# Kernel tuning notes

Measured on AMD Instinct MI355X. Metric: run time of the kernel, lower is better.

The kernel has to match this reference:

```python
import jax, jax.numpy as jnp
import numpy as np

N_NODES = 100000


def gcn_layer(x, W, b, src, dst, n):
    # PyG GCNConv: h = x @ W, then D^{-1/2}(A+I)D^{-1/2} aggregation, then + b
    h = x @ W  # [N, out]
    ones = jnp.ones(src.shape[0], dtype=h.dtype)
    deg = jax.ops.segment_sum(ones, dst, num_segments=n) + 1.0  # +1 for self loop
    dinv = jax.lax.rsqrt(deg)  # [N]
    norm = dinv[src] * dinv[dst]  # [E]
    msgs = h[src] * norm[:, None]  # gather + scale, [E, out]
    agg = jax.ops.segment_sum(msgs, dst, num_segments=n)
    agg = agg + h * (dinv * dinv)[:, None]  # self-loop term
    return agg + b


def setup_inputs() -> dict:
    key = jax.random.key(0)
    k1, k2, k3, k4, k5, k6 = jax.random.split(key, 6)
    in_dim, h1, h2 = 256, 128, 64
    x = jax.random.normal(k1, (N_NODES, in_dim), dtype=jnp.float32)
    edge_index = jax.random.randint(k2, (2, 1600000), 0, N_NODES, dtype=jnp.int64)
    # Glorot-style init for weights, zeros for bias (PyG default)
    W1 = jax.random.normal(k3, (in_dim, h1), dtype=jnp.float32) / np.sqrt(in_dim)
    b1 = jnp.zeros((h1,), dtype=jnp.float32)
    W2 = jax.random.normal(k4, (h1, h2), dtype=jnp.float32) / np.sqrt(h1)
    b2 = jnp.zeros((h2,), dtype=jnp.float32)
    return {"x": x, "W1": W1, "b1": b1, "W2": W2, "b2": b2, "edge_index": edge_index}


def reference(x, W1, b1, W2, b2, edge_index):
    src, dst = edge_index[0], edge_index[1]
    n = x.shape[0]
    h = jax.nn.relu(gcn_layer(x, W1, b1, src, dst, n))
    h = jax.nn.relu(gcn_layer(h, W2, b2, src, dst, n))
    return h
```

## Files before the change

### kernel.cpp

```cpp
#include <hip/hip_runtime.h>
#include <hip/hip_bf16.h>


typedef __attribute__((ext_vector_type(8))) short bf16x8;
typedef __attribute__((ext_vector_type(4))) float f32x4;

__device__ inline unsigned short f2bf(float f) {
    unsigned u = __float_as_uint(f);
    u = (u + 0x7fff + ((u >> 16) & 1)) >> 16;
    return (unsigned short)u;
}
__device__ inline float bf2f(unsigned short h) {
    return __uint_as_float(((unsigned)h) << 16);
}
__device__ inline float bflo(unsigned u) { return __uint_as_float(u << 16); }
__device__ inline float bfhi(unsigned u) { return __uint_as_float(u & 0xffff0000u); }
__device__ inline unsigned pack_bf16_2(float lo, float hi) {
    return (unsigned)f2bf(lo) | ((unsigned)f2bf(hi) << 16);
}
__device__ inline void cvt8(const float* v, bf16x8& h8, bf16x8& l8) {
    #pragma unroll
    for (int j = 0; j < 8; ++j) {
        unsigned short h = f2bf(v[j]);
        h8[j] = (short)h;
        l8[j] = (short)f2bf(v[j] - bf2f(h));
    }
}

__global__ void prep_kernel(const int* __restrict__ dst, int* __restrict__ deg, int E,
        const float* __restrict__ W1, unsigned short* __restrict__ w1h,
        unsigned short* __restrict__ w1l,
        const float* __restrict__ W2, unsigned short* __restrict__ w2h,
        unsigned short* __restrict__ w2l) {
    const int W1B = (256 * 128) / 256;
    const int W2B = (128 * 64) / 256;
    int b = blockIdx.x;
    if (b < W1B) {
        int idx = b * 256 + threadIdx.x;
        int k = idx >> 7, n = idx & 127;
        float v = W1[idx];
        unsigned short h = f2bf(v);
        w1h[(size_t)n * 256 + k] = h;
        w1l[(size_t)n * 256 + k] = f2bf(v - bf2f(h));
    } else if (b < W1B + W2B) {
        int idx = (b - W1B) * 256 + threadIdx.x;
        int k = idx >> 6, n = idx & 63;
        float v = W2[idx];
        unsigned short h = f2bf(v);
        w2h[(size_t)n * 128 + k] = h;
        w2l[(size_t)n * 128 + k] = f2bf(v - bf2f(h));
    } else {
        int nb = gridDim.x - (W1B + W2B);
        int stride = nb * 256;
        for (int i = (b - W1B - W2B) * 256 + threadIdx.x; i < E; i += stride)
            atomicAdd(&deg[dst[i]], 1);
    }
}

__global__ __launch_bounds__(1024) void scan_partial_kernel(const int* __restrict__ deg,
        int* __restrict__ psum, float* __restrict__ dinv, int n) {
    __shared__ int wsum[16];
    int tid = threadIdx.x, wave = tid >> 6, lane = tid & 63;
    int i0 = blockIdx.x * 4096 + tid * 4;
    int v0 = 0, v1 = 0, v2 = 0, v3 = 0;
    if (i0 + 3 < n) {
        int4 v = *(const int4*)(deg + i0);
        v0 = v.x; v1 = v.y; v2 = v.z; v3 = v.w;
    } else {
        if (i0 + 0 < n) v0 = deg[i0 + 0];
        if (i0 + 1 < n) v1 = deg[i0 + 1];
        if (i0 + 2 < n) v2 = deg[i0 + 2];
        if (i0 + 3 < n) v3 = deg[i0 + 3];
    }
    if (i0 + 0 < n) dinv[i0 + 0] = 1.0f / sqrtf((float)v0 + 1.0f);
    if (i0 + 1 < n) dinv[i0 + 1] = 1.0f / sqrtf((float)v1 + 1.0f);
    if (i0 + 2 < n) dinv[i0 + 2] = 1.0f / sqrtf((float)v2 + 1.0f);
    if (i0 + 3 < n) dinv[i0 + 3] = 1.0f / sqrtf((float)v3 + 1.0f);
    int s = v0 + v1 + v2 + v3;
    #pragma unroll
    for (int off = 1; off < 64; off <<= 1) s += __shfl_xor(s, off, 64);
    if (lane == 0) wsum[wave] = s;
    __syncthreads();
    if (tid == 0) {
        int t = 0;
        #pragma unroll
        for (int w = 0; w < 16; ++w) t += wsum[w];
        psum[blockIdx.x] = t;
    }
}

__global__ __launch_bounds__(1024) void scan_local_kernel(const int* __restrict__ deg,
        const int* __restrict__ psum, int* __restrict__ offs, int n, int sb) {
    __shared__ int wsum[16];
    int tid = threadIdx.x, wave = tid >> 6, lane = tid & 63;
    int bid = blockIdx.x;
    int base = 0, total = 0;
    for (int w = 0; w < sb; ++w) {
        int t = psum[w];
        if (w < bid) base += t;
        total += t;
    }
    if (bid == 0 && tid == 0) offs[n] = total;

    int i0 = bid * 4096 + tid * 4;
    int v0 = 0, v1 = 0, v2 = 0, v3 = 0;
    if (i0 + 3 < n) {
        int4 v = *(const int4*)(deg + i0);
        v0 = v.x; v1 = v.y; v2 = v.z; v3 = v.w;
    } else {
        if (i0 + 0 < n) v0 = deg[i0 + 0];
        if (i0 + 1 < n) v1 = deg[i0 + 1];
        if (i0 + 2 < n) v2 = deg[i0 + 2];
        if (i0 + 3 < n) v3 = deg[i0 + 3];
    }
    int s = v0 + v1 + v2 + v3;
    int x = s;
    #pragma unroll
    for (int off = 1; off < 64; off <<= 1) {
        int y = __shfl_up(x, off, 64);
        if (lane >= off) x += y;
    }
    if (lane == 63) wsum[wave] = x;
    __syncthreads();
    int wbase = 0;
    #pragma unroll
    for (int w = 0; w < 16; ++w)
        if (w < wave) wbase += wsum[w];
    int ex = base + wbase + (x - s);
    if (i0 + 0 < n) offs[i0 + 0] = ex;
    if (i0 + 1 < n) offs[i0 + 1] = ex + v0;
    if (i0 + 2 < n) offs[i0 + 2] = ex + v0 + v1;
    if (i0 + 3 < n) offs[i0 + 3] = ex + v0 + v1 + v2;
}

__global__ __launch_bounds__(256) void fused_fill_gemm1(
        const int* __restrict__ src, const int* __restrict__ dst,
        const int* __restrict__ offs, int* __restrict__ cursor,
        int* __restrict__ csr, int E, int NG,
        const float* __restrict__ X,
        const unsigned short* __restrict__ Wh, const unsigned short* __restrict__ Wl,
        const float* __restrict__ dinv, unsigned short* __restrict__ G, int M) {
    const int bid2 = blockIdx.x >> 1;
    if (!(blockIdx.x & 1)) {
        int stride = NG * 256;
        for (int i = bid2 * 256 + threadIdx.x; i < E; i += stride) {
            int d = dst[i];
            int pos = offs[d] + atomicAdd(&cursor[d], 1);
            csr[pos] = src[i];
        }
        return;
    }
    constexpr int K = 256;
    const int tid = threadIdx.x;
    const int wv = tid >> 6, ln = tid & 63;
    const int l16 = ln & 15, kseg = ln >> 4;
    const int r0 = bid2 * 128 + wv * 32;

    int rA0 = r0 + l16;       if (rA0 >= M) rA0 = M - 1;
    int rA1 = r0 + 16 + l16;  if (rA1 >= M) rA1 = M - 1;
    const float* pA0 = X + (size_t)rA0 * K + kseg * 8;
    const float* pA1 = X + (size_t)rA1 * K + kseg * 8;

    f32x4 acc[2][8];
    #pragma unroll
    for (int a = 0; a < 2; ++a)
        #pragma unroll
        for (int b = 0; b < 8; ++b) acc[a][b] = 0;

    #pragma unroll 2
    for (int k0 = 0; k0 < K; k0 += 32) {
        bf16x8 ah[2], al[2];
        {
            float4 qa = *(const float4*)(pA0 + k0);
            float4 qb = *(const float4*)(pA0 + k0 + 4);
            float v[8] = {qa.x, qa.y, qa.z, qa.w, qb.x, qb.y, qb.z, qb.w};
            cvt8(v, ah[0], al[0]);
        }
        {
            float4 qa = *(const float4*)(pA1 + k0);
            float4 qb = *(const float4*)(pA1 + k0 + 4);
            float v[8] = {qa.x, qa.y, qa.z, qa.w, qb.x, qb.y, qb.z, qb.w};
            cvt8(v, ah[1], al[1]);
        }
        #pragma unroll
        for (int tc = 0; tc < 8; ++tc) {
            size_t wo = (size_t)(tc * 16 + l16) * K + k0 + kseg * 8;
            bf16x8 bh = *(const bf16x8*)(Wh + wo);
            bf16x8 bl = *(const bf16x8*)(Wl + wo);
            #pragma unroll
            for (int tr = 0; tr < 2; ++tr) {
                acc[tr][tc] = __builtin_amdgcn_mfma_f32_16x16x32_bf16(ah[tr], bh, acc[tr][tc], 0, 0, 0);
                acc[tr][tc] = __builtin_amdgcn_mfma_f32_16x16x32_bf16(al[tr], bh, acc[tr][tc], 0, 0, 0);
                acc[tr][tc] = __builtin_amdgcn_mfma_f32_16x16x32_bf16(ah[tr], bl, acc[tr][tc], 0, 0, 0);
            }
        }
    }

    #pragma unroll
    for (int tr = 0; tr < 2; ++tr) {
        int rbase = r0 + tr * 16 + (ln >> 4) * 4;
        #pragma unroll
        for (int r = 0; r < 4; ++r) {
            int row = rbase + r;
            if (row < M) {
                float dv = dinv[row];
                #pragma unroll
                for (int tc = 0; tc < 8; ++tc)
                    G[(size_t)row * 128 + tc * 16 + l16] = f2bf(acc[tr][tc][r] * dv);
            }
        }
    }
}

__global__ __launch_bounds__(256) void gemm2_kernel(const unsigned short* __restrict__ H,
        const unsigned short* __restrict__ Wh, const unsigned short* __restrict__ Wl,
        const float* __restrict__ dinv, unsigned short* __restrict__ G, int M) {
    constexpr int K = 128;
    const int tid = threadIdx.x;
    const int wv = tid >> 6, ln = tid & 63;
    const int l16 = ln & 15, kseg = ln >> 4;
    const int r0 = blockIdx.x * 128 + wv * 32;

    int rA0 = r0 + l16;       if (rA0 >= M) rA0 = M - 1;
    int rA1 = r0 + 16 + l16;  if (rA1 >= M) rA1 = M - 1;
    const unsigned short* pA0 = H + (size_t)rA0 * K + kseg * 8;
    const unsigned short* pA1 = H + (size_t)rA1 * K + kseg * 8;

    f32x4 acc[2][4];
    #pragma unroll
    for (int a = 0; a < 2; ++a)
        #pragma unroll
        for (int b = 0; b < 4; ++b) acc[a][b] = 0;

    #pragma unroll
    for (int k0 = 0; k0 < K; k0 += 32) {
        bf16x8 a0 = *(const bf16x8*)(pA0 + k0);
        bf16x8 a1 = *(const bf16x8*)(pA1 + k0);
        #pragma unroll
        for (int tc = 0; tc < 4; ++tc) {
            size_t wo = (size_t)(tc * 16 + l16) * K + k0 + kseg * 8;
            bf16x8 bh = *(const bf16x8*)(Wh + wo);
            bf16x8 bl = *(const bf16x8*)(Wl + wo);
            acc[0][tc] = __builtin_amdgcn_mfma_f32_16x16x32_bf16(a0, bh, acc[0][tc], 0, 0, 0);
            acc[0][tc] = __builtin_amdgcn_mfma_f32_16x16x32_bf16(a0, bl, acc[0][tc], 0, 0, 0);
            acc[1][tc] = __builtin_amdgcn_mfma_f32_16x16x32_bf16(a1, bh, acc[1][tc], 0, 0, 0);
            acc[1][tc] = __builtin_amdgcn_mfma_f32_16x16x32_bf16(a1, bl, acc[1][tc], 0, 0, 0);
        }
    }

    #pragma unroll
    for (int tr = 0; tr < 2; ++tr) {
        int rbase = r0 + tr * 16 + (ln >> 4) * 4;
        #pragma unroll
        for (int r = 0; r < 4; ++r) {
            int row = rbase + r;
            if (row < M) {
                float dv = dinv[row];
                #pragma unroll
                for (int tc = 0; tc < 4; ++tc)
                    G[(size_t)row * 64 + tc * 16 + l16] = f2bf(acc[tr][tc][r] * dv);
            }
        }
    }
}

__global__ __launch_bounds__(256) void aggregate128_kernel(const unsigned* __restrict__ G,
        const int* __restrict__ csr, const int* __restrict__ offs,
        const float* __restrict__ dinv, const float* __restrict__ bias,
        unsigned* __restrict__ out, int n) {
    int wave = threadIdx.x >> 6, lane = threadIdx.x & 63;
    int node = blockIdx.x * 4 + wave;
    if (node >= n) return;
    int beg = offs[node], end = offs[node + 1];

    unsigned u = G[(size_t)node * 64 + lane];
    float a0 = bflo(u), a1 = bfhi(u);
    int e = beg;
    for (; e + 4 <= end; e += 4) {
        int s0 = csr[e], s1 = csr[e + 1], s2 = csr[e + 2], s3 = csr[e + 3];
        unsigned u0 = G[(size_t)s0 * 64 + lane];
        unsigned u1 = G[(size_t)s1 * 64 + lane];
        unsigned u2 = G[(size_t)s2 * 64 + lane];
        unsigned u3 = G[(size_t)s3 * 64 + lane];
        a0 += (bflo(u0) + bflo(u1)) + (bflo(u2) + bflo(u3));
        a1 += (bfhi(u0) + bfhi(u1)) + (bfhi(u2) + bfhi(u3));
    }
    for (; e < end; ++e) {
        unsigned u0 = G[(size_t)csr[e] * 64 + lane];
        a0 += bflo(u0);
        a1 += bfhi(u0);
    }
    float di = dinv[node];
    float rx = fmaxf(fmaf(a0, di, bias[lane * 2 + 0]), 0.0f);
    float ry = fmaxf(fmaf(a1, di, bias[lane * 2 + 1]), 0.0f);
    out[(size_t)node * 64 + lane] = pack_bf16_2(rx, ry);
}

__global__ __launch_bounds__(256) void aggregate64_kernel(const unsigned* __restrict__ G,
        const int* __restrict__ csr, const int* __restrict__ offs,
        const float* __restrict__ dinv, const float* __restrict__ bias,
        float* __restrict__ out, int n) {
    int wave = threadIdx.x >> 6, lane = threadIdx.x & 63;
    int node = blockIdx.x * 4 + wave;
    if (node >= n) return;
    int beg = offs[node], end = offs[node + 1];
    int half = lane >> 5, col = lane & 31;

    float a0 = 0.0f, a1 = 0.0f;
    if (half == 0) {
        unsigned u = G[(size_t)node * 32 + col];
        a0 = bflo(u); a1 = bfhi(u);
    }
    int e = beg;
    for (; e + 4 <= end; e += 4) {
        int sA = csr[e + half], sB = csr[e + 2 + half];
        unsigned uA = G[(size_t)sA * 32 + col];
        unsigned uB = G[(size_t)sB * 32 + col];
        a0 += bflo(uA) + bflo(uB);
        a1 += bfhi(uA) + bfhi(uB);
    }
    if (e + 2 <= end) {
        int sA = csr[e + half];
        unsigned uA = G[(size_t)sA * 32 + col];
        a0 += bflo(uA);
        a1 += bfhi(uA);
        e += 2;
    }
    if (e < end && half == 0) {
        unsigned uA = G[(size_t)csr[e] * 32 + col];
        a0 += bflo(uA);
        a1 += bfhi(uA);
    }
    a0 += __shfl_down(a0, 32, 64);
    a1 += __shfl_down(a1, 32, 64);
    if (half == 0) {
        float di = dinv[node];
        float2 r;
        r.x = fmaxf(fmaf(a0, di, bias[col * 2 + 0]), 0.0f);
        r.y = fmaxf(fmaf(a1, di, bias[col * 2 + 1]), 0.0f);
        ((float2*)(out + (size_t)node * 64))[col] = r;
    }
}

extern "C" void kernel_launch(void* const* d_in, const int* in_sizes, int n_in,
                              void* d_out, int out_size, void* d_ws, size_t ws_size,
                              hipStream_t stream) {
    const float* x  = (const float*)d_in[0];
    const float* W1 = (const float*)d_in[1];
    const float* b1 = (const float*)d_in[2];
    const float* W2 = (const float*)d_in[3];
    const float* b2 = (const float*)d_in[4];
    const int* edge = (const int*)d_in[5];

    const int IN = 256, H1 = 128, H2 = 64;
    const int E = in_sizes[5] / 2;
    const int N = in_sizes[0] / IN;
    const int* srcp = edge;
    const int* dstp = edge + E;

    char* ws = (char*)d_ws;
    auto alignup = [](size_t v) { return (v + 255) & ~(size_t)255; };
    size_t off = 0;
    size_t degSz = alignup((size_t)N * 4);
    int*            deg    = (int*)(ws + off);            off += degSz;
    int*            cursor = (int*)(ws + off);            off += degSz;
    int*            offs   = (int*)(ws + off);            off += alignup(((size_t)N + 1) * 4);
    float*          dinv   = (float*)(ws + off);          off += degSz;
    int*            psum   = (int*)(ws + off);            off += alignup(64 * 4);
    int*            csr    = (int*)(ws + off);            off += alignup((size_t)E * 4);
    unsigned short* wt1h   = (unsigned short*)(ws + off); off += alignup((size_t)IN * H1 * 2);
    unsigned short* wt1l   = (unsigned short*)(ws + off); off += alignup((size_t)IN * H1 * 2);
    unsigned short* wt2h   = (unsigned short*)(ws + off); off += alignup((size_t)H1 * H2 * 2);
    unsigned short* wt2l   = (unsigned short*)(ws + off); off += alignup((size_t)H1 * H2 * 2);
    unsigned short* g1     = (unsigned short*)(ws + off); off += alignup((size_t)N * H1 * 2);
    unsigned*       h1b    = (unsigned*)(ws + off);       off += alignup((size_t)N * (H1 / 2) * 4);
    unsigned short* g2     = g1;

    hipMemsetAsync(deg, 0, 2 * degSz, stream);

    int hgrid = 2048;
    int sb = (N + 4095) / 4096;

    prep_kernel<<<160 + hgrid, 256, 0, stream>>>(dstp, deg, E, W1, wt1h, wt1l,
                                                 W2, wt2h, wt2l);
    scan_partial_kernel<<<sb, 1024, 0, stream>>>(deg, psum, dinv, N);
    scan_local_kernel<<<sb, 1024, 0, stream>>>(deg, psum, offs, N, sb);

    const int NG = (N + 127) / 128;
    fused_fill_gemm1<<<2 * NG, 256, 0, stream>>>(srcp, dstp, offs, cursor, csr, E,
                                                 NG, x, wt1h, wt1l, dinv, g1, N);

    int agrid = (N + 3) / 4;
    aggregate128_kernel<<<agrid, 256, 0, stream>>>((const unsigned*)g1, csr, offs,
                                                   dinv, b1, h1b, N);
    gemm2_kernel<<<NG, 256, 0, stream>>>((const unsigned short*)h1b, wt2h, wt2l,
                                         dinv, g2, N);
    aggregate64_kernel<<<agrid, 256, 0, stream>>>((const unsigned*)g2, csr, offs,
                                                  dinv, b2, (float*)d_out, N);
}
```

Before: 544.0 us.

## Split fill from GEMM1, shrink GEMM tiles, deepen aggregation gather unroll

The fused CSR-fill and GEMM1 kernel becomes two kernels: a grid-stride fill kernel and a separate GEMM1. The GEMM1 block tile drops to 64 rows, with waves split across column halves and A loads prefetched one k-step ahead. GEMM2 also uses 64-row blocks with one 16-row tile per wave. Both aggregation kernels issue 8 neighbor gathers per iteration to raise memory-level parallelism. This gives up the overlap between fill atomics and GEMM compute in exchange for more blocks and better latency hiding, and adds one extra launch.

```diff
diff --git a/kernel.cpp b/kernel.cpp
--- a/kernel.cpp
+++ b/kernel.cpp
@@ -133,58 +133,63 @@
     if (i0 + 3 < n) offs[i0 + 3] = ex + v0 + v1 + v2;
 }
 
-__global__ __launch_bounds__(256) void fused_fill_gemm1(
-        const int* __restrict__ src, const int* __restrict__ dst,
+__global__ void fill_kernel(const int* __restrict__ src, const int* __restrict__ dst,
         const int* __restrict__ offs, int* __restrict__ cursor,
-        int* __restrict__ csr, int E, int NG,
-        const float* __restrict__ X,
+        int* __restrict__ csr, int E) {
+    int stride = gridDim.x * blockDim.x;
+    for (int i = blockIdx.x * blockDim.x + threadIdx.x; i < E; i += stride) {
+        int d = dst[i];
+        int pos = offs[d] + atomicAdd(&cursor[d], 1);
+        csr[pos] = src[i];
+    }
+}
+
+__global__ __launch_bounds__(256) void gemm1_kernel(const float* __restrict__ X,
         const unsigned short* __restrict__ Wh, const unsigned short* __restrict__ Wl,
         const float* __restrict__ dinv, unsigned short* __restrict__ G, int M) {
-    const int bid2 = blockIdx.x >> 1;
-    if (!(blockIdx.x & 1)) {
-        int stride = NG * 256;
-        for (int i = bid2 * 256 + threadIdx.x; i < E; i += stride) {
-            int d = dst[i];
-            int pos = offs[d] + atomicAdd(&cursor[d], 1);
-            csr[pos] = src[i];
-        }
-        return;
-    }
     constexpr int K = 256;
     const int tid = threadIdx.x;
     const int wv = tid >> 6, ln = tid & 63;
     const int l16 = ln & 15, kseg = ln >> 4;
-    const int r0 = bid2 * 128 + wv * 32;
+    const int wr = wv >> 1, wc = wv & 1;
+    const int r0 = blockIdx.x * 64 + wr * 32;
 
     int rA0 = r0 + l16;       if (rA0 >= M) rA0 = M - 1;
     int rA1 = r0 + 16 + l16;  if (rA1 >= M) rA1 = M - 1;
     const float* pA0 = X + (size_t)rA0 * K + kseg * 8;
     const float* pA1 = X + (size_t)rA1 * K + kseg * 8;
 
-    f32x4 acc[2][8];
+    f32x4 acc[2][4];
     #pragma unroll
     for (int a = 0; a < 2; ++a)
         #pragma unroll
-        for (int b = 0; b < 8; ++b) acc[a][b] = 0;
+        for (int b = 0; b < 4; ++b) acc[a][b] = 0;
+
+    float4 qa0 = *(const float4*)(pA0);
+    float4 qb0 = *(const float4*)(pA0 + 4);
+    float4 qa1 = *(const float4*)(pA1);
+    float4 qb1 = *(const float4*)(pA1 + 4);
 
     #pragma unroll 2
     for (int k0 = 0; k0 < K; k0 += 32) {
         bf16x8 ah[2], al[2];
         {
-            float4 qa = *(const float4*)(pA0 + k0);
-            float4 qb = *(const float4*)(pA0 + k0 + 4);
-            float v[8] = {qa.x, qa.y, qa.z, qa.w, qb.x, qb.y, qb.z, qb.w};
+            float v[8] = {qa0.x, qa0.y, qa0.z, qa0.w, qb0.x, qb0.y, qb0.z, qb0.w};
             cvt8(v, ah[0], al[0]);
         }
         {
-            float4 qa = *(const float4*)(pA1 + k0);
-            float4 qb = *(const float4*)(pA1 + k0 + 4);
-            float v[8] = {qa.x, qa.y, qa.z, qa.w, qb.x, qb.y, qb.z, qb.w};
+            float v[8] = {qa1.x, qa1.y, qa1.z, qa1.w, qb1.x, qb1.y, qb1.z, qb1.w};
             cvt8(v, ah[1], al[1]);
         }
-        #pragma unroll
-        for (int tc = 0; tc < 8; ++tc) {
-            size_t wo = (size_t)(tc * 16 + l16) * K + k0 + kseg * 8;
+        if (k0 + 32 < K) {
+            qa0 = *(const float4*)(pA0 + k0 + 32);
+            qb0 = *(const float4*)(pA0 + k0 + 36);
+            qa1 = *(const float4*)(pA1 + k0 + 32);
+            qb1 = *(const float4*)(pA1 + k0 + 36);
+        }
+        #pragma unroll
+        for (int tc = 0; tc < 4; ++tc) {
+            size_t wo = (size_t)(wc * 64 + tc * 16 + l16) * K + k0 + kseg * 8;
             bf16x8 bh = *(const bf16x8*)(Wh + wo);
             bf16x8 bl = *(const bf16x8*)(Wl + wo);
             #pragma unroll
@@ -205,8 +210,9 @@
             if (row < M) {
                 float dv = dinv[row];
                 #pragma unroll
-                for (int tc = 0; tc < 8; ++tc)
-                    G[(size_t)row * 128 + tc * 16 + l16] = f2bf(acc[tr][tc][r] * dv);
+                for (int tc = 0; tc < 4; ++tc)
+                    G[(size_t)row * 128 + wc * 64 + tc * 16 + l16] =
+                        f2bf(acc[tr][tc][r] * dv);
             }
         }
     }
@@ -219,38 +225,30 @@
     const int tid = threadIdx.x;
     const int wv = tid >> 6, ln = tid & 63;
     const int l16 = ln & 15, kseg = ln >> 4;
-    const int r0 = blockIdx.x * 128 + wv * 32;
-
-    int rA0 = r0 + l16;       if (rA0 >= M) rA0 = M - 1;
-    int rA1 = r0 + 16 + l16;  if (rA1 >= M) rA1 = M - 1;
+    const int r0 = blockIdx.x * 64 + wv * 16;
+
+    int rA0 = r0 + l16;  if (rA0 >= M) rA0 = M - 1;
     const unsigned short* pA0 = H + (size_t)rA0 * K + kseg * 8;
-    const unsigned short* pA1 = H + (size_t)rA1 * K + kseg * 8;
-
-    f32x4 acc[2][4];
-    #pragma unroll
-    for (int a = 0; a < 2; ++a)
-        #pragma unroll
-        for (int b = 0; b < 4; ++b) acc[a][b] = 0;
+
+    f32x4 acc[4];
+    #pragma unroll
+    for (int b = 0; b < 4; ++b) acc[b] = 0;
 
     #pragma unroll
     for (int k0 = 0; k0 < K; k0 += 32) {
         bf16x8 a0 = *(const bf16x8*)(pA0 + k0);
-        bf16x8 a1 = *(const bf16x8*)(pA1 + k0);
         #pragma unroll
         for (int tc = 0; tc < 4; ++tc) {
             size_t wo = (size_t)(tc * 16 + l16) * K + k0 + kseg * 8;
             bf16x8 bh = *(const bf16x8*)(Wh + wo);
             bf16x8 bl = *(const bf16x8*)(Wl + wo);
-            acc[0][tc] = __builtin_amdgcn_mfma_f32_16x16x32_bf16(a0, bh, acc[0][tc], 0, 0, 0);
-            acc[0][tc] = __builtin_amdgcn_mfma_f32_16x16x32_bf16(a0, bl, acc[0][tc], 0, 0, 0);
-            acc[1][tc] = __builtin_amdgcn_mfma_f32_16x16x32_bf16(a1, bh, acc[1][tc], 0, 0, 0);
-            acc[1][tc] = __builtin_amdgcn_mfma_f32_16x16x32_bf16(a1, bl, acc[1][tc], 0, 0, 0);
-        }
-    }
-
-    #pragma unroll
-    for (int tr = 0; tr < 2; ++tr) {
-        int rbase = r0 + tr * 16 + (ln >> 4) * 4;
+            acc[tc] = __builtin_amdgcn_mfma_f32_16x16x32_bf16(a0, bh, acc[tc], 0, 0, 0);
+            acc[tc] = __builtin_amdgcn_mfma_f32_16x16x32_bf16(a0, bl, acc[tc], 0, 0, 0);
+        }
+    }
+
+    {
+        int rbase = r0 + (ln >> 4) * 4;
         #pragma unroll
         for (int r = 0; r < 4; ++r) {
             int row = rbase + r;
@@ -258,7 +256,7 @@
                 float dv = dinv[row];
                 #pragma unroll
                 for (int tc = 0; tc < 4; ++tc)
-                    G[(size_t)row * 64 + tc * 16 + l16] = f2bf(acc[tr][tc][r] * dv);
+                    G[(size_t)row * 64 + tc * 16 + l16] = f2bf(acc[tc][r] * dv);
             }
         }
     }
@@ -276,14 +274,19 @@
     unsigned u = G[(size_t)node * 64 + lane];
     float a0 = bflo(u), a1 = bfhi(u);
     int e = beg;
+    for (; e + 8 <= end; e += 8) {
+        unsigned uu[8];
+        #pragma unroll
+        for (int j = 0; j < 8; ++j) uu[j] = G[(size_t)csr[e + j] * 64 + lane];
+        #pragma unroll
+        for (int j = 0; j < 8; ++j) { a0 += bflo(uu[j]); a1 += bfhi(uu[j]); }
+    }
     for (; e + 4 <= end; e += 4) {
-        int s0 = csr[e], s1 = csr[e + 1], s2 = csr[e + 2], s3 = csr[e + 3];
-        unsigned u0 = G[(size_t)s0 * 64 + lane];
-        unsigned u1 = G[(size_t)s1 * 64 + lane];
-        unsigned u2 = G[(size_t)s2 * 64 + lane];
-        unsigned u3 = G[(size_t)s3 * 64 + lane];
-        a0 += (bflo(u0) + bflo(u1)) + (bflo(u2) + bflo(u3));
-        a1 += (bfhi(u0) + bfhi(u1)) + (bfhi(u2) + bfhi(u3));
+        unsigned uu[4];
+        #pragma unroll
+        for (int j = 0; j < 4; ++j) uu[j] = G[(size_t)csr[e + j] * 64 + lane];
+        #pragma unroll
+        for (int j = 0; j < 4; ++j) { a0 += bflo(uu[j]); a1 += bfhi(uu[j]); }
     }
     for (; e < end; ++e) {
         unsigned u0 = G[(size_t)csr[e] * 64 + lane];
@@ -312,19 +315,17 @@
         a0 = bflo(u); a1 = bfhi(u);
     }
     int e = beg;
-    for (; e + 4 <= end; e += 4) {
-        int sA = csr[e + half], sB = csr[e + 2 + half];
-        unsigned uA = G[(size_t)sA * 32 + col];
-        unsigned uB = G[(size_t)sB * 32 + col];
-        a0 += bflo(uA) + bflo(uB);
-        a1 += bfhi(uA) + bfhi(uB);
-    }
-    if (e + 2 <= end) {
-        int sA = csr[e + half];
-        unsigned uA = G[(size_t)sA * 32 + col];
+    for (; e + 8 <= end; e += 8) {
+        unsigned uu[4];
+        #pragma unroll
+        for (int j = 0; j < 4; ++j) uu[j] = G[(size_t)csr[e + 2 * j + half] * 32 + col];
+        #pragma unroll
+        for (int j = 0; j < 4; ++j) { a0 += bflo(uu[j]); a1 += bfhi(uu[j]); }
+    }
+    for (; e + 2 <= end; e += 2) {
+        unsigned uA = G[(size_t)csr[e + half] * 32 + col];
         a0 += bflo(uA);
         a1 += bfhi(uA);
-        e += 2;
     }
     if (e < end && half == 0) {
         unsigned uA = G[(size_t)csr[e] * 32 + col];
@@ -378,23 +379,22 @@
 
     hipMemsetAsync(deg, 0, 2 * degSz, stream);
 
-    int hgrid = 2048;
     int sb = (N + 4095) / 4096;
 
-    prep_kernel<<<160 + hgrid, 256, 0, stream>>>(dstp, deg, E, W1, wt1h, wt1l,
-                                                 W2, wt2h, wt2l);
+    prep_kernel<<<160 + 2048, 256, 0, stream>>>(dstp, deg, E, W1, wt1h, wt1l,
+                                                W2, wt2h, wt2l);
     scan_partial_kernel<<<sb, 1024, 0, stream>>>(deg, psum, dinv, N);
     scan_local_kernel<<<sb, 1024, 0, stream>>>(deg, psum, offs, N, sb);
-
-    const int NG = (N + 127) / 128;
-    fused_fill_gemm1<<<2 * NG, 256, 0, stream>>>(srcp, dstp, offs, cursor, csr, E,
-                                                 NG, x, wt1h, wt1l, dinv, g1, N);
-
+    fill_kernel<<<1024, 256, 0, stream>>>(srcp, dstp, offs, cursor, csr, E);
+
+    int g64 = (N + 63) / 64;
     int agrid = (N + 3) / 4;
+
+    gemm1_kernel<<<g64, 256, 0, stream>>>(x, wt1h, wt1l, dinv, g1, N);
     aggregate128_kernel<<<agrid, 256, 0, stream>>>((const unsigned*)g1, csr, offs,
                                                    dinv, b1, h1b, N);
-    gemm2_kernel<<<NG, 256, 0, stream>>>((const unsigned short*)h1b, wt2h, wt2l,
-                                         dinv, g2, N);
+    gemm2_kernel<<<g64, 256, 0, stream>>>((const unsigned short*)h1b, wt2h, wt2l,
+                                          dinv, g2, N);
     aggregate64_kernel<<<agrid, 256, 0, stream>>>((const unsigned*)g2, csr, offs,
                                                   dinv, b2, (float*)d_out, N);
 }
```

Measured after the change: 534.1 us. Within noise of the previous version (-1.8%).
